# Kernel optimization log

Measured on AMD Instinct MI355X. Metric: run time of the kernel, lower is better.

The kernel has to match this reference:

```python
import jax, jax.numpy as jnp
import numpy as np

V, E, H, L, T, B = 50257, 1024, 16, 12, 128, 16
FF = 4 * E
STD = 0.02


def setup_inputs() -> dict:
    key = jax.random.key(0)
    ks = jax.random.split(key, 20)
    n = lambda k, shape: (jax.random.normal(k, shape, dtype=jnp.float32) * STD)
    inp = {
        'idx': jax.random.randint(ks[0], (B, T), 0, V, dtype=jnp.int64),
        'targets': jax.random.randint(ks[1], (B, T), 0, V, dtype=jnp.int64),
        'tok_emb': n(ks[2], (V, E)),
        'pos_emb': n(ks[3], (T, E)),
        'wq': n(ks[4], (L, E, E)),
        'wk': n(ks[5], (L, E, E)),
        'wv': n(ks[6], (L, E, E)),
        'w_proj': n(ks[7], (L, E, E)),
        'b_proj': jnp.zeros((L, E), jnp.float32),
        'ln1_g': jnp.ones((L, E), jnp.float32),
        'ln1_b': jnp.zeros((L, E), jnp.float32),
        'ln2_g': jnp.ones((L, E), jnp.float32),
        'ln2_b': jnp.zeros((L, E), jnp.float32),
        'w_fc1': n(ks[8], (L, E, FF)),
        'b_fc1': jnp.zeros((L, FF), jnp.float32),
        'w_fc2': n(ks[9], (L, FF, E)),
        'b_fc2': jnp.zeros((L, E), jnp.float32),
        'lnf_g': jnp.ones((E,), jnp.float32),
        'lnf_b': jnp.zeros((E,), jnp.float32),
        'w_head': n(ks[10], (E, V)),
        'b_head': jnp.zeros((V,), jnp.float32),
    }
    return inp


def _layernorm(x, g, b, eps=1e-5):
    m = x.mean(-1, keepdims=True)
    v = ((x - m) ** 2).mean(-1, keepdims=True)
    return (x - m) / jnp.sqrt(v + eps) * g + b


def _forward(idx, targets, tok_emb, pos_emb, wq, wk, wv, w_proj, b_proj,
             ln1_g, ln1_b, ln2_g, ln2_b, w_fc1, b_fc1, w_fc2, b_fc2,
             lnf_g, lnf_b, w_head, b_head):
    Bb, Tt = idx.shape
    x = tok_emb[idx] + pos_emb[:Tt]  # (B, T, E)
    causal = jnp.tril(jnp.ones((Tt, Tt), dtype=bool))
    scale = E ** (-0.5)  # NOTE: original scales by full n_embd, not head_size

    def block(x, p):
        (wq_l, wk_l, wv_l, wp_l, bp_l, g1, b1, g2, b2, wf1, bf1, wf2, bf2) = p
        h = _layernorm(x, g1, b1)
        q = (h @ wq_l).reshape(Bb, Tt, H, -1)
        k = (h @ wk_l).reshape(Bb, Tt, H, -1)
        v = (h @ wv_l).reshape(Bb, Tt, H, -1)
        sc = jnp.einsum('bthd,bshd->bhts', q, k) * scale
        sc = jnp.where(causal, sc, -jnp.inf)
        att = jax.nn.softmax(sc, axis=-1)
        o = jnp.einsum('bhts,bshd->bthd', att, v).reshape(Bb, Tt, E)
        x = x + o @ wp_l + bp_l
        h2 = _layernorm(x, g2, b2)
        x = x + jax.nn.relu(h2 @ wf1 + bf1) @ wf2 + bf2
        return x, None

    x, _ = jax.lax.scan(block, x, (wq, wk, wv, w_proj, b_proj, ln1_g, ln1_b,
                                   ln2_g, ln2_b, w_fc1, b_fc1, w_fc2, b_fc2))
    x = _layernorm(x, lnf_g, lnf_b)
    logits = x @ w_head + b_head  # (B, T, V)
    logp = jax.nn.log_softmax(logits, axis=-1)
    nll = -jnp.take_along_axis(logp.reshape(Bb * Tt, -1),
                               targets.reshape(-1, 1), axis=1)
    loss = nll.mean()
    return logits, loss


def reference(idx, targets, tok_emb, pos_emb, wq, wk, wv, w_proj, b_proj,
              ln1_g, ln1_b, ln2_g, ln2_b, w_fc1, b_fc1, w_fc2, b_fc2,
              lnf_g, lnf_b, w_head, b_head):
    return _forward(idx, targets, tok_emb, pos_emb, wq, wk, wv, w_proj, b_proj,
                    ln1_g, ln1_b, ln2_g, ln2_b, w_fc1, b_fc1, w_fc2, b_fc2,
                    lnf_g, lnf_b, w_head, b_head)
```

## Files before the change

### kernel.cpp

```cpp
#include <hip/hip_runtime.h>
#include <math.h>

typedef unsigned short u16;
typedef float f32x4 __attribute__((ext_vector_type(4)));
typedef short bf16x8 __attribute__((ext_vector_type(8)));
typedef unsigned short us4 __attribute__((ext_vector_type(4)));

#define DEVI __device__ __forceinline__

DEVI float bf2f(u16 u) { return __uint_as_float(((unsigned int)u) << 16); }
DEVI u16 f2bf(float f) {
    unsigned int u = __float_as_uint(f);
    u += 0x7fffu + ((u >> 16) & 1u);
    return (u16)(u >> 16);
}

__global__ __launch_bounds__(256) void k_embed(const int* __restrict__ idx,
                                               const float* __restrict__ te,
                                               const float* __restrict__ pe,
                                               float* __restrict__ x) {
    int m = blockIdx.x;
    int t = m & 127;
    int tok = idx[m];
    const f32x4* a = (const f32x4*)(te + (long)tok * 1024);
    const f32x4* p = (const f32x4*)(pe + (long)t * 1024);
    f32x4* o = (f32x4*)(x + (long)m * 1024);
    o[threadIdx.x] = a[threadIdx.x] + p[threadIdx.x];
}

__global__ __launch_bounds__(256) void k_ln(const float* __restrict__ x,
                                            const float* __restrict__ g,
                                            const float* __restrict__ b,
                                            u16* __restrict__ out) {
    __shared__ float red[8];
    int tid = threadIdx.x, lane = tid & 63, wid = tid >> 6;
    int r = blockIdx.x;
    f32x4 v = ((const f32x4*)(x + (long)r * 1024))[tid];
    float s = v.x + v.y + v.z + v.w;
#pragma unroll
    for (int o2 = 32; o2; o2 >>= 1) s += __shfl_xor(s, o2);
    if (lane == 0) red[wid] = s;
    __syncthreads();
    float mean = (red[0] + red[1] + red[2] + red[3]) * (1.0f / 1024.0f);
    f32x4 d; d.x = v.x - mean; d.y = v.y - mean; d.z = v.z - mean; d.w = v.w - mean;
    float sq = d.x * d.x + d.y * d.y + d.z * d.z + d.w * d.w;
#pragma unroll
    for (int o2 = 32; o2; o2 >>= 1) sq += __shfl_xor(sq, o2);
    if (lane == 0) red[4 + wid] = sq;
    __syncthreads();
    float rstd = rsqrtf((red[4] + red[5] + red[6] + red[7]) * (1.0f / 1024.0f) + 1e-5f);
    f32x4 gg = ((const f32x4*)g)[tid];
    f32x4 bb = ((const f32x4*)b)[tid];
    us4 o4;
    o4.x = f2bf(d.x * rstd * gg.x + bb.x);
    o4.y = f2bf(d.y * rstd * gg.y + bb.y);
    o4.z = f2bf(d.z * rstd * gg.z + bb.z);
    o4.w = f2bf(d.w * rstd * gg.w + bb.w);
    ((us4*)(out + (long)r * 1024))[tid] = o4;
}

DEVI void tr_tile(const float* __restrict__ in, u16* __restrict__ out,
                  int K, int N, int k0, int n0, int tid, float (*tile)[65]) {
    int trow = tid >> 4;
    int tcol = (tid & 15) * 4;
#pragma unroll
    for (int p = 0; p < 4; ++p) {
        int k = k0 + trow + p * 16;
        const float* src = in + (long)k * N + n0 + tcol;
#pragma unroll
        for (int j = 0; j < 4; ++j) {
            int n = n0 + tcol + j;
            tile[trow + p * 16][tcol + j] = (n < N) ? src[j] : 0.0f;
        }
    }
    __syncthreads();
#pragma unroll
    for (int p = 0; p < 4; ++p) {
        int n = n0 + trow + p * 16;
        if (n < N) {
            us4 o4;
#pragma unroll
            for (int j = 0; j < 4; ++j) o4[j] = f2bf(tile[tcol + j][trow + p * 16]);
            *(us4*)(out + (long)n * K + k0 + tcol) = o4;
        }
    }
}

__global__ __launch_bounds__(256) void k_tr_one(const float* __restrict__ in,
                                                u16* __restrict__ out, int K, int N) {
    __shared__ float tile[64][65];
    tr_tile(in, out, K, N, blockIdx.y * 64, blockIdx.x * 64, threadIdx.x, tile);
}

__global__ __launch_bounds__(256) void k_tr_layer(
    const float* __restrict__ wq, const float* __restrict__ wk,
    const float* __restrict__ wv, const float* __restrict__ wp,
    const float* __restrict__ f1, const float* __restrict__ f2,
    u16* __restrict__ oqkv, u16* __restrict__ oproj,
    u16* __restrict__ of1, u16* __restrict__ of2) {
    __shared__ float tile[64][65];
    int id = blockIdx.x;
    const float* in; u16* out; int K, N, txx, tyy;
    if (id < 1024) {
        int t = id >> 8, s2 = id & 255;
        txx = s2 & 15; tyy = s2 >> 4; K = 1024; N = 1024;
        in = (t == 0) ? wq : (t == 1) ? wk : (t == 2) ? wv : wp;
        out = (t == 3) ? oproj : oqkv + (long)t * 1024 * 1024;
    } else if (id < 2048) {
        int s2 = id - 1024;
        txx = s2 & 63; tyy = s2 >> 6; K = 1024; N = 4096; in = f1; out = of1;
    } else {
        int s2 = id - 2048;
        txx = s2 & 15; tyy = s2 >> 4; K = 4096; N = 1024; in = f2; out = of2;
    }
    tr_tile(in, out, K, N, tyy * 64, txx * 64, threadIdx.x, tile);
}

template <int ROWS>
DEVI void stage_tile(const u16* __restrict__ g, long row0, long rowmax, int ld,
                     int col0, char* lds, int tid) {
    constexpr int NCH = ROWS * 8;
#pragma unroll
    for (int p = 0; p < NCH / 256; ++p) {
        int c = tid + p * 256;
        int row = c >> 3;
        int gslot = c & 7;
        int gdata = gslot ^ (row & 7);
        long gr = row0 + row;
        if (gr > rowmax) gr = rowmax;
        const u16* src = g + gr * (long)ld + col0 + gdata * 8;
        char* dst = lds + ((long)((tid & 192) + p * 256)) * 16;
        __builtin_amdgcn_global_load_lds(
            (const __attribute__((address_space(1))) void*)src,
            (__attribute__((address_space(3))) void*)dst, 16, 0, 0);
    }
}

template <int ROWS>
DEVI void stage512(const u16* __restrict__ g, long row0, long rowmax, int ld,
                   int col0, char* lds, int tid) {
    constexpr int NP = ROWS * 8 / 512;
#pragma unroll
    for (int p = 0; p < NP; ++p) {
        int c = tid + p * 512;
        int row = c >> 3;
        int gslot = c & 7;
        int gdata = gslot ^ (row & 7);
        long gr = row0 + row;
        if (gr > rowmax) gr = rowmax;
        const u16* src = g + gr * (long)ld + col0 + gdata * 8;
        char* dst = lds + ((long)((tid & 448) + p * 512)) * 16;
        __builtin_amdgcn_global_load_lds(
            (const __attribute__((address_space(1))) void*)src,
            (__attribute__((address_space(3))) void*)dst, 16, 0, 0);
    }
}

template <int BN, bool OUT_BF16, bool RELU, bool HAS_BIAS, bool HAS_RES>
__global__ __launch_bounds__(256, 2) void k_gemm(
    const u16* __restrict__ A, const u16* __restrict__ Bt,
    const float* __restrict__ bias, const float* __restrict__ res,
    float* __restrict__ Cf, u16* __restrict__ Cb,
    int M, int N, int K, int ldc) {
    constexpr int NR = BN / 32;
    constexpr int ASZ = 128 * 64 * 2;
    constexpr int BSZ = BN * 64 * 2;
    __shared__ __align__(16) char lds[2 * (ASZ + BSZ)];
    int tid = threadIdx.x, lane = tid & 63, wid = tid >> 6;
    int l15 = lane & 15, l4 = lane >> 4;
    int wr = wid >> 1, wc = wid & 1;
    long m0 = (long)blockIdx.y * 128;
    long n0 = (long)blockIdx.x * BN;
    f32x4 acc[4][NR] = {};
    const int nk = K >> 6;

    stage_tile<128>(A, m0, (long)M - 1, K, 0, lds, tid);
    stage_tile<BN>(Bt, n0, (long)N - 1, K, 0, lds + ASZ, tid);
    int cur = 0;
    for (int kt = 0; kt < nk; ++kt) {
        __syncthreads();
        if (kt + 1 < nk) {
            char* nb = lds + (cur ^ 1) * (ASZ + BSZ);
            stage_tile<128>(A, m0, (long)M - 1, K, (kt + 1) << 6, nb, tid);
            stage_tile<BN>(Bt, n0, (long)N - 1, K, (kt + 1) << 6, nb + ASZ, tid);
        }
        const char* ab = lds + cur * (ASZ + BSZ);
        const char* bb = ab + ASZ;
#pragma unroll
        for (int kh = 0; kh < 2; ++kh) {
            bf16x8 af[4], bfv[NR];
#pragma unroll
            for (int mi = 0; mi < 4; ++mi) {
                int row = wr * 64 + mi * 16 + l15;
                int slot = (kh * 4 + l4) ^ (row & 7);
                af[mi] = *(const bf16x8*)(ab + (row * 8 + slot) * 16);
            }
#pragma unroll
            for (int ni = 0; ni < NR; ++ni) {
                int row = wc * (BN / 2) + ni * 16 + l15;
                int slot = (kh * 4 + l4) ^ (row & 7);
                bfv[ni] = *(const bf16x8*)(bb + (row * 8 + slot) * 16);
            }
#pragma unroll
            for (int mi = 0; mi < 4; ++mi)
#pragma unroll
                for (int ni = 0; ni < NR; ++ni)
                    acc[mi][ni] = __builtin_amdgcn_mfma_f32_16x16x32_bf16(
                        af[mi], bfv[ni], acc[mi][ni], 0, 0, 0);
        }
        cur ^= 1;
    }
#pragma unroll
    for (int ni = 0; ni < NR; ++ni) {
        long n = n0 + wc * (BN / 2) + ni * 16 + l15;
        if (n < N) {
            float bv = HAS_BIAS ? bias[n] : 0.0f;
#pragma unroll
            for (int mi = 0; mi < 4; ++mi) {
#pragma unroll
                for (int j = 0; j < 4; ++j) {
                    long m = m0 + wr * 64 + mi * 16 + l4 * 4 + j;
                    float v = acc[mi][ni][j] + bv;
                    if (HAS_RES) v += res[m * (long)ldc + n];
                    if (RELU) v = fmaxf(v, 0.0f);
                    if (OUT_BF16) Cb[m * (long)ldc + n] = f2bf(v);
                    else Cf[m * (long)ldc + n] = v;
                }
            }
        }
    }
}

__global__ __launch_bounds__(512, 2) void k_gemm_head(
    const u16* __restrict__ A, const u16* __restrict__ Bt,
    const float* __restrict__ bias, float* __restrict__ Cf,
    float2* __restrict__ part, int M, int N, int K, int ldc, int ncb) {
    constexpr int TSZ = 256 * 64 * 2;
    __shared__ __align__(16) char lds[4 * TSZ];
    __shared__ float pmx[4][256], psm[4][256];
    int tid = threadIdx.x, lane = tid & 63, wid = tid >> 6;
    int l15 = lane & 15, l4 = lane >> 4;
    int wr = wid >> 2, wc = wid & 3;
    int bm = blockIdx.x & 7, bn = blockIdx.x >> 3;
    long m0 = (long)bm * 256, n0 = (long)bn * 256;
    const int nk = K >> 6;
    f32x4 acc[8][4] = {};

    stage512<256>(A, m0, (long)M - 1, K, 0, lds, tid);
    stage512<256>(Bt, n0, (long)N - 1, K, 0, lds + TSZ, tid);
    stage512<256>(A, m0, (long)M - 1, K, 64, lds + 2 * TSZ, tid);
    stage512<256>(Bt, n0, (long)N - 1, K, 64, lds + 3 * TSZ, tid);

    for (int t = 0; t < nk; ++t) {
        if (t < nk - 1) asm volatile("s_waitcnt vmcnt(8)" ::: "memory");
        else            asm volatile("s_waitcnt vmcnt(0)" ::: "memory");
        __builtin_amdgcn_s_barrier();
        const char* ab = lds + (t & 1) * 2 * TSZ;
        const char* bb = ab + TSZ;
#pragma unroll
        for (int kh = 0; kh < 2; ++kh) {
            bf16x8 af[8], bfv[4];
#pragma unroll
            for (int mi = 0; mi < 8; ++mi) {
                int row = wr * 128 + mi * 16 + l15;
                int slot = (kh * 4 + l4) ^ (row & 7);
                af[mi] = *(const bf16x8*)(ab + (row * 8 + slot) * 16);
            }
#pragma unroll
            for (int ni = 0; ni < 4; ++ni) {
                int row = wc * 64 + ni * 16 + l15;
                int slot = (kh * 4 + l4) ^ (row & 7);
                bfv[ni] = *(const bf16x8*)(bb + (row * 8 + slot) * 16);
            }
            __builtin_amdgcn_s_setprio(1);
#pragma unroll
            for (int mi = 0; mi < 8; ++mi)
#pragma unroll
                for (int ni = 0; ni < 4; ++ni)
                    acc[mi][ni] = __builtin_amdgcn_mfma_f32_16x16x32_bf16(
                        af[mi], bfv[ni], acc[mi][ni], 0, 0, 0);
            __builtin_amdgcn_s_setprio(0);
        }
        __builtin_amdgcn_s_barrier();
        if (t + 2 < nk) {
            char* na = lds + (t & 1) * 2 * TSZ;
            stage512<256>(A, m0, (long)M - 1, K, (t + 2) << 6, na, tid);
            stage512<256>(Bt, n0, (long)N - 1, K, (t + 2) << 6, na + TSZ, tid);
        }
    }
    const float BIG_NEG = -1e30f;
    float bvv[4];
#pragma unroll
    for (int ni = 0; ni < 4; ++ni) {
        long n = n0 + wc * 64 + ni * 16 + l15;
        bvv[ni] = (n < N) ? bias[n] : 0.0f;
    }
#pragma unroll
    for (int mi = 0; mi < 8; ++mi) {
#pragma unroll
        for (int j = 0; j < 4; ++j) {
            int rloc = wr * 128 + mi * 16 + l4 * 4 + j;
            long m = m0 + rloc;
            float mx = BIG_NEG, vv[4];
#pragma unroll
            for (int ni = 0; ni < 4; ++ni) {
                long n = n0 + wc * 64 + ni * 16 + l15;
                float v = acc[mi][ni][j] + bvv[ni];
                if (n < N) Cf[m * (long)ldc + n] = v;
                else v = BIG_NEG;
                vv[ni] = v;
                mx = fmaxf(mx, v);
            }
#pragma unroll
            for (int ofs = 1; ofs < 16; ofs <<= 1) mx = fmaxf(mx, __shfl_xor(mx, ofs));
            float sm = 0.f;
#pragma unroll
            for (int ni = 0; ni < 4; ++ni) sm += __expf(vv[ni] - mx);
#pragma unroll
            for (int ofs = 1; ofs < 16; ofs <<= 1) sm += __shfl_xor(sm, ofs);
            if (l15 == 0) { pmx[wc][rloc] = mx; psm[wc][rloc] = sm; }
        }
    }
    __syncthreads();
    if (tid < 256) {
        float Mv = pmx[0][tid], Sv = psm[0][tid];
#pragma unroll
        for (int q = 1; q < 4; ++q) {
            float m2 = pmx[q][tid], s2 = psm[q][tid];
            float nm = fmaxf(Mv, m2);
            Sv = Sv * __expf(Mv - nm) + s2 * __expf(m2 - nm);
            Mv = nm;
        }
        part[(m0 + tid) * (long)ncb + bn] = make_float2(Mv, Sv);
    }
}

__global__ __launch_bounds__(256) void k_attn_mfma(const u16* __restrict__ qkv,
                                                   u16* __restrict__ o) {
    __shared__ __align__(16) u16 Ks[128 * 64];
    __shared__ __align__(16) u16 Vt[64 * 128];
    __shared__ __align__(16) u16 Ps[4][32 * 128];
    int tid = threadIdx.x, lane = tid & 63, w = tid >> 6;
    int l15 = lane & 15, l4 = lane >> 4;
    int b = blockIdx.x >> 4, h = blockIdx.x & 15;
    const u16* base = qkv + (long)b * 128 * 3072 + h * 64;

    stage_tile<128>(base + 1024, 0, 127, 3072, 0, (char*)Ks, tid);
    {
        const u16* vg = base + 2048;
#pragma unroll
        for (int p = 0; p < 4; ++p) {
            int s0 = (w * 4 + p) * 8;
            u16 tmp[8];
#pragma unroll
            for (int j = 0; j < 8; ++j) tmp[j] = vg[(long)(s0 + j) * 3072 + lane];
            int slot = (s0 >> 3) ^ (lane & 7);
            *(bf16x8*)((char*)Vt + lane * 256 + slot * 16) = *(bf16x8*)tmp;
        }
    }
    bf16x8 aq[2][2];
#pragma unroll
    for (int mj = 0; mj < 2; ++mj)
#pragma unroll
        for (int kk = 0; kk < 2; ++kk)
            aq[mj][kk] = *(const bf16x8*)(base + (long)(w * 32 + mj * 16 + l15) * 3072 + kk * 32 + l4 * 8);
    __syncthreads();

    f32x4 sacc[2][8] = {};
#pragma unroll
    for (int sj = 0; sj < 8; ++sj) {
        bf16x8 bk[2];
#pragma unroll
        for (int kk = 0; kk < 2; ++kk) {
            int row = sj * 16 + l15;
            int slot = (kk * 4 + l4) ^ (row & 7);
            bk[kk] = *(const bf16x8*)((char*)Ks + (row * 8 + slot) * 16);
        }
#pragma unroll
        for (int mj = 0; mj < 2; ++mj) {
            sacc[mj][sj] = __builtin_amdgcn_mfma_f32_16x16x32_bf16(aq[mj][0], bk[0], sacc[mj][sj], 0, 0, 0);
            sacc[mj][sj] = __builtin_amdgcn_mfma_f32_16x16x32_bf16(aq[mj][1], bk[1], sacc[mj][sj], 0, 0, 0);
        }
    }
    const float scale = 0.03125f;
#pragma unroll
    for (int mj = 0; mj < 2; ++mj) {
#pragma unroll
        for (int j = 0; j < 4; ++j) {
            int tq = w * 32 + mj * 16 + l4 * 4 + j;
            float mx = -INFINITY;
#pragma unroll
            for (int sj = 0; sj < 8; ++sj) {
                int s = sj * 16 + l15;
                float v = (s <= tq) ? sacc[mj][sj][j] * scale : -INFINITY;
                sacc[mj][sj][j] = v;
                mx = fmaxf(mx, v);
            }
#pragma unroll
            for (int ofs = 1; ofs < 16; ofs <<= 1) mx = fmaxf(mx, __shfl_xor(mx, ofs));
            float sm = 0.f;
#pragma unroll
            for (int sj = 0; sj < 8; ++sj) {
                float e = __expf(sacc[mj][sj][j] - mx);
                sacc[mj][sj][j] = e;
                sm += e;
            }
#pragma unroll
            for (int ofs = 1; ofs < 16; ofs <<= 1) sm += __shfl_xor(sm, ofs);
            float inv = 1.0f / sm;
            int m2 = mj * 16 + l4 * 4 + j;
            u16* prow = Ps[w] + m2 * 128;
#pragma unroll
            for (int sj = 0; sj < 8; ++sj) {
                int s = sj * 16 + l15;
                int slot = (s >> 3) ^ (m2 & 7);
                prow[slot * 8 + (s & 7)] = f2bf(sacc[mj][sj][j] * inv);
            }
        }
    }
    f32x4 oacc[2][4] = {};
#pragma unroll
    for (int kk = 0; kk < 4; ++kk) {
        bf16x8 pa[2], bv[4];
#pragma unroll
        for (int mj = 0; mj < 2; ++mj) {
            int m2 = mj * 16 + l15;
            int slot = (kk * 4 + l4) ^ (m2 & 7);
            pa[mj] = *(const bf16x8*)((char*)(Ps[w]) + m2 * 256 + slot * 16);
        }
#pragma unroll
        for (int nb = 0; nb < 4; ++nb) {
            int d = nb * 16 + l15;
            int slot = (kk * 4 + l4) ^ (d & 7);
            bv[nb] = *(const bf16x8*)((char*)Vt + d * 256 + slot * 16);
        }
#pragma unroll
        for (int mj = 0; mj < 2; ++mj)
#pragma unroll
            for (int nb = 0; nb < 4; ++nb)
                oacc[mj][nb] = __builtin_amdgcn_mfma_f32_16x16x32_bf16(pa[mj], bv[nb], oacc[mj][nb], 0, 0, 0);
    }
#pragma unroll
    for (int mj = 0; mj < 2; ++mj)
#pragma unroll
        for (int nb = 0; nb < 4; ++nb) {
            int d = nb * 16 + l15;
#pragma unroll
            for (int j = 0; j < 4; ++j) {
                int tq = w * 32 + mj * 16 + l4 * 4 + j;
                o[((long)b * 128 + tq) * 1024 + h * 64 + d] = f2bf(oacc[mj][nb][j]);
            }
        }
}

__global__ __launch_bounds__(64) void k_loss_rows2(const float2* __restrict__ part,
                                                   const float* __restrict__ logits,
                                                   const int* __restrict__ tgt,
                                                   float* __restrict__ rowloss, int ncb) {
    int r = blockIdx.x, lane = threadIdx.x;
    float M = -1e30f, S = 0.f;
    for (int cb = lane; cb < ncb; cb += 64) {
        float2 p = part[(long)r * ncb + cb];
        float nm = fmaxf(M, p.x);
        S = S * __expf(M - nm) + p.y * __expf(p.x - nm);
        M = nm;
    }
#pragma unroll
    for (int ofs = 32; ofs; ofs >>= 1) {
        float M2 = __shfl_xor(M, ofs), S2 = __shfl_xor(S, ofs);
        float nm = fmaxf(M, M2);
        S = S * __expf(M - nm) + S2 * __expf(M2 - nm);
        M = nm;
    }
    if (lane == 0)
        rowloss[r] = (M + logf(S)) - logits[(long)r * 50257 + tgt[r]];
}

__global__ __launch_bounds__(256) void k_loss_reduce(const float* __restrict__ rowloss,
                                                     float* __restrict__ out) {
    __shared__ float red[4];
    int tid = threadIdx.x, lane = tid & 63, wid = tid >> 6;
    float s = 0.f;
    for (int i = tid; i < 2048; i += 256) s += rowloss[i];
#pragma unroll
    for (int ofs = 32; ofs; ofs >>= 1) s += __shfl_xor(s, ofs);
    if (lane == 0) red[wid] = s;
    __syncthreads();
    if (tid == 0) out[0] = (red[0] + red[1] + red[2] + red[3]) * (1.0f / 2048.0f);
}

extern "C" void kernel_launch(void* const* d_in, const int* in_sizes, int n_in,
                              void* d_out, int out_size, void* d_ws, size_t ws_size,
                              hipStream_t stream) {
    (void)in_sizes; (void)n_in; (void)out_size; (void)ws_size;
    const int*   idx     = (const int*)d_in[0];
    const int*   targets = (const int*)d_in[1];
    const float* tok_emb = (const float*)d_in[2];
    const float* pos_emb = (const float*)d_in[3];
    const float* wq      = (const float*)d_in[4];
    const float* wk      = (const float*)d_in[5];
    const float* wv      = (const float*)d_in[6];
    const float* w_proj  = (const float*)d_in[7];
    const float* b_proj  = (const float*)d_in[8];
    const float* ln1_g   = (const float*)d_in[9];
    const float* ln1_b   = (const float*)d_in[10];
    const float* ln2_g   = (const float*)d_in[11];
    const float* ln2_b   = (const float*)d_in[12];
    const float* w_fc1   = (const float*)d_in[13];
    const float* b_fc1   = (const float*)d_in[14];
    const float* w_fc2   = (const float*)d_in[15];
    const float* b_fc2   = (const float*)d_in[16];
    const float* lnf_g   = (const float*)d_in[17];
    const float* lnf_b   = (const float*)d_in[18];
    const float* w_head  = (const float*)d_in[19];
    const float* b_head  = (const float*)d_in[20];
    float* out = (float*)d_out;

    char* w = (char*)d_ws;
    auto alloc = [&](size_t bytes) {
        char* p = w;
        w += (bytes + 255) & ~(size_t)255;
        return p;
    };
    u16*    wT_qkv  = (u16*)alloc(3072L * 1024 * 2);
    u16*    wT_proj = (u16*)alloc(1024L * 1024 * 2);
    u16*    wT_f1   = (u16*)alloc(4096L * 1024 * 2);
    u16*    wT_f2   = (u16*)alloc(1024L * 4096 * 2);
    u16*    wT_head = (u16*)alloc(50257L * 1024 * 2);
    float*  x       = (float*)alloc(2048L * 1024 * 4);
    u16*    h_bf    = (u16*)alloc(2048L * 1024 * 2);
    u16*    qkvb    = (u16*)alloc(2048L * 3072 * 2);
    u16*    o_bf    = (u16*)alloc(2048L * 1024 * 2);
    u16*    ff_bf   = (u16*)alloc(2048L * 4096 * 2);
    float2* part    = (float2*)alloc(2048L * 197 * 8);
    float*  rowloss = (float*)alloc(2048L * 4);

    k_embed<<<2048, 256, 0, stream>>>(idx, tok_emb, pos_emb, x);
    k_tr_one<<<dim3(786, 16), 256, 0, stream>>>(w_head, wT_head, 1024, 50257);

    for (int l = 0; l < 12; ++l) {
        k_tr_layer<<<3072, 256, 0, stream>>>(
            wq + (long)l * 1048576, wk + (long)l * 1048576,
            wv + (long)l * 1048576, w_proj + (long)l * 1048576,
            w_fc1 + (long)l * 4194304, w_fc2 + (long)l * 4194304,
            wT_qkv, wT_proj, wT_f1, wT_f2);
        k_ln<<<2048, 256, 0, stream>>>(x, ln1_g + l * 1024, ln1_b + l * 1024, h_bf);
        k_gemm<64, true, false, false, false><<<dim3(48, 16), 256, 0, stream>>>(
            h_bf, wT_qkv, nullptr, nullptr, nullptr, qkvb, 2048, 3072, 1024, 3072);
        k_attn_mfma<<<256, 256, 0, stream>>>(qkvb, o_bf);
        k_gemm<64, false, false, true, true><<<dim3(16, 16), 256, 0, stream>>>(
            o_bf, wT_proj, b_proj + l * 1024, x, x, nullptr, 2048, 1024, 1024, 1024);
        k_ln<<<2048, 256, 0, stream>>>(x, ln2_g + l * 1024, ln2_b + l * 1024, h_bf);
        k_gemm<128, true, true, true, false><<<dim3(32, 16), 256, 0, stream>>>(
            h_bf, wT_f1, b_fc1 + l * 4096, nullptr, nullptr, ff_bf, 2048, 4096, 1024, 4096);
        k_gemm<64, false, false, true, true><<<dim3(16, 16), 256, 0, stream>>>(
            ff_bf, wT_f2, b_fc2 + l * 1024, x, x, nullptr, 2048, 1024, 4096, 1024);
    }
    k_ln<<<2048, 256, 0, stream>>>(x, lnf_g, lnf_b, h_bf);
    k_gemm_head<<<1576, 512, 0, stream>>>(h_bf, wT_head, b_head, out, part,
                                          2048, 50257, 1024, 50257, 197);
    k_loss_rows2<<<2048, 64, 0, stream>>>(part, out, targets, rowloss, 197);
    k_loss_reduce<<<1, 256, 0, stream>>>(rowloss, out + 102926336L);
}
```

Before: 2.158 ms.

## Shrink head GEMM tiles to 128x128 with XCD-aware block ordering

Replaces the 256x256-tile, 512-thread LM-head GEMM with a 128x128-tile, 256-thread kernel that uses the single-buffer-ahead staging from the layer GEMM. Block indices are remapped so each XCD handles a contiguous range of N column blocks across all 16 M blocks, which is meant to improve L2 reuse of head weight columns. The change raises the block count to improve occupancy and load balance. In exchange, per-tile arithmetic intensity is lower, A and B are re-read from memory more often, and the online-softmax partials grow to 400 per row, which makes the loss kernel do more work. The grid pads N to 400 blocks (50 per XCD), so some blocks past N do clamped redundant loads.

```diff
diff --git a/kernel.cpp b/kernel.cpp
--- a/kernel.cpp
+++ b/kernel.cpp
@@ -136,26 +136,6 @@
     }
 }
 
-template <int ROWS>
-DEVI void stage512(const u16* __restrict__ g, long row0, long rowmax, int ld,
-                   int col0, char* lds, int tid) {
-    constexpr int NP = ROWS * 8 / 512;
-#pragma unroll
-    for (int p = 0; p < NP; ++p) {
-        int c = tid + p * 512;
-        int row = c >> 3;
-        int gslot = c & 7;
-        int gdata = gslot ^ (row & 7);
-        long gr = row0 + row;
-        if (gr > rowmax) gr = rowmax;
-        const u16* src = g + gr * (long)ld + col0 + gdata * 8;
-        char* dst = lds + ((long)((tid & 448) + p * 512)) * 16;
-        __builtin_amdgcn_global_load_lds(
-            (const __attribute__((address_space(1))) void*)src,
-            (__attribute__((address_space(3))) void*)dst, 16, 0, 0);
-    }
-}
-
 template <int BN, bool OUT_BF16, bool RELU, bool HAS_BIAS, bool HAS_RES>
 __global__ __launch_bounds__(256, 2) void k_gemm(
     const u16* __restrict__ A, const u16* __restrict__ Bt,
@@ -231,38 +211,43 @@
     }
 }
 
-__global__ __launch_bounds__(512, 2) void k_gemm_head(
+__global__ __launch_bounds__(256, 2) void k_head128(
     const u16* __restrict__ A, const u16* __restrict__ Bt,
     const float* __restrict__ bias, float* __restrict__ Cf,
     float2* __restrict__ part, int M, int N, int K, int ldc, int ncb) {
-    constexpr int TSZ = 256 * 64 * 2;
-    __shared__ __align__(16) char lds[4 * TSZ];
-    __shared__ float pmx[4][256], psm[4][256];
+    constexpr int ASZ = 128 * 64 * 2;
+    constexpr int BSZ = 128 * 64 * 2;
+    __shared__ __align__(16) char lds[2 * (ASZ + BSZ)];
+    __shared__ float pmx[2][128], psm[2][128];
     int tid = threadIdx.x, lane = tid & 63, wid = tid >> 6;
     int l15 = lane & 15, l4 = lane >> 4;
-    int wr = wid >> 2, wc = wid & 3;
-    int bm = blockIdx.x & 7, bn = blockIdx.x >> 3;
-    long m0 = (long)bm * 256, n0 = (long)bn * 256;
+    int wr = wid >> 1, wc = wid & 1;
+    int id = blockIdx.x;
+    int xcd = id & 7, s = id >> 3;
+    int bn = xcd * 50 + (s >> 4);
+    int bm = s & 15;
+    long m0 = (long)bm * 128, n0 = (long)bn * 128;
+    f32x4 acc[4][4] = {};
     const int nk = K >> 6;
-    f32x4 acc[8][4] = {};
-
-    stage512<256>(A, m0, (long)M - 1, K, 0, lds, tid);
-    stage512<256>(Bt, n0, (long)N - 1, K, 0, lds + TSZ, tid);
-    stage512<256>(A, m0, (long)M - 1, K, 64, lds + 2 * TSZ, tid);
-    stage512<256>(Bt, n0, (long)N - 1, K, 64, lds + 3 * TSZ, tid);
-
-    for (int t = 0; t < nk; ++t) {
-        if (t < nk - 1) asm volatile("s_waitcnt vmcnt(8)" ::: "memory");
-        else            asm volatile("s_waitcnt vmcnt(0)" ::: "memory");
-        __builtin_amdgcn_s_barrier();
-        const char* ab = lds + (t & 1) * 2 * TSZ;
-        const char* bb = ab + TSZ;
+
+    stage_tile<128>(A, m0, (long)M - 1, K, 0, lds, tid);
+    stage_tile<128>(Bt, n0, (long)N - 1, K, 0, lds + ASZ, tid);
+    int cur = 0;
+    for (int kt = 0; kt < nk; ++kt) {
+        __syncthreads();
+        if (kt + 1 < nk) {
+            char* nb = lds + (cur ^ 1) * (ASZ + BSZ);
+            stage_tile<128>(A, m0, (long)M - 1, K, (kt + 1) << 6, nb, tid);
+            stage_tile<128>(Bt, n0, (long)N - 1, K, (kt + 1) << 6, nb + ASZ, tid);
+        }
+        const char* ab = lds + cur * (ASZ + BSZ);
+        const char* bb = ab + ASZ;
 #pragma unroll
         for (int kh = 0; kh < 2; ++kh) {
-            bf16x8 af[8], bfv[4];
-#pragma unroll
-            for (int mi = 0; mi < 8; ++mi) {
-                int row = wr * 128 + mi * 16 + l15;
+            bf16x8 af[4], bfv[4];
+#pragma unroll
+            for (int mi = 0; mi < 4; ++mi) {
+                int row = wr * 64 + mi * 16 + l15;
                 int slot = (kh * 4 + l4) ^ (row & 7);
                 af[mi] = *(const bf16x8*)(ab + (row * 8 + slot) * 16);
             }
@@ -272,21 +257,14 @@
                 int slot = (kh * 4 + l4) ^ (row & 7);
                 bfv[ni] = *(const bf16x8*)(bb + (row * 8 + slot) * 16);
             }
-            __builtin_amdgcn_s_setprio(1);
-#pragma unroll
-            for (int mi = 0; mi < 8; ++mi)
+#pragma unroll
+            for (int mi = 0; mi < 4; ++mi)
 #pragma unroll
                 for (int ni = 0; ni < 4; ++ni)
                     acc[mi][ni] = __builtin_amdgcn_mfma_f32_16x16x32_bf16(
                         af[mi], bfv[ni], acc[mi][ni], 0, 0, 0);
-            __builtin_amdgcn_s_setprio(0);
-        }
-        __builtin_amdgcn_s_barrier();
-        if (t + 2 < nk) {
-            char* na = lds + (t & 1) * 2 * TSZ;
-            stage512<256>(A, m0, (long)M - 1, K, (t + 2) << 6, na, tid);
-            stage512<256>(Bt, n0, (long)N - 1, K, (t + 2) << 6, na + TSZ, tid);
-        }
+        }
+        cur ^= 1;
     }
     const float BIG_NEG = -1e30f;
     float bvv[4];
@@ -296,10 +274,10 @@
         bvv[ni] = (n < N) ? bias[n] : 0.0f;
     }
 #pragma unroll
-    for (int mi = 0; mi < 8; ++mi) {
+    for (int mi = 0; mi < 4; ++mi) {
 #pragma unroll
         for (int j = 0; j < 4; ++j) {
-            int rloc = wr * 128 + mi * 16 + l4 * 4 + j;
+            int rloc = wr * 64 + mi * 16 + l4 * 4 + j;
             long m = m0 + rloc;
             float mx = BIG_NEG, vv[4];
 #pragma unroll
@@ -322,16 +300,11 @@
         }
     }
     __syncthreads();
-    if (tid < 256) {
-        float Mv = pmx[0][tid], Sv = psm[0][tid];
-#pragma unroll
-        for (int q = 1; q < 4; ++q) {
-            float m2 = pmx[q][tid], s2 = psm[q][tid];
-            float nm = fmaxf(Mv, m2);
-            Sv = Sv * __expf(Mv - nm) + s2 * __expf(m2 - nm);
-            Mv = nm;
-        }
-        part[(m0 + tid) * (long)ncb + bn] = make_float2(Mv, Sv);
+    if (tid < 128) {
+        float m1 = pmx[0][tid], m2 = pmx[1][tid];
+        float nm = fmaxf(m1, m2);
+        float S = psm[0][tid] * __expf(m1 - nm) + psm[1][tid] * __expf(m2 - nm);
+        part[(m0 + tid) * (long)ncb + bn] = make_float2(nm, S);
     }
 }
 
@@ -532,7 +505,7 @@
     u16*    qkvb    = (u16*)alloc(2048L * 3072 * 2);
     u16*    o_bf    = (u16*)alloc(2048L * 1024 * 2);
     u16*    ff_bf   = (u16*)alloc(2048L * 4096 * 2);
-    float2* part    = (float2*)alloc(2048L * 197 * 8);
+    float2* part    = (float2*)alloc(2048L * 400 * 8);
     float*  rowloss = (float*)alloc(2048L * 4);
 
     k_embed<<<2048, 256, 0, stream>>>(idx, tok_emb, pos_emb, x);
@@ -557,8 +530,8 @@
             ff_bf, wT_f2, b_fc2 + l * 1024, x, x, nullptr, 2048, 1024, 4096, 1024);
     }
     k_ln<<<2048, 256, 0, stream>>>(x, lnf_g, lnf_b, h_bf);
-    k_gemm_head<<<1576, 512, 0, stream>>>(h_bf, wT_head, b_head, out, part,
-                                          2048, 50257, 1024, 50257, 197);
-    k_loss_rows2<<<2048, 64, 0, stream>>>(part, out, targets, rowloss, 197);
+    k_head128<<<6400, 256, 0, stream>>>(h_bf, wT_head, b_head, out, part,
+                                        2048, 50257, 1024, 50257, 400);
+    k_loss_rows2<<<2048, 64, 0, stream>>>(part, out, targets, rowloss, 400);
     k_loss_reduce<<<1, 256, 0, stream>>>(rowloss, out + 102926336L);
 }
```

Measured after the change: 2.213 ms. +2.5%, slower.
